# Optimization experiments

Hardware: AMD Instinct MI355X
Metric: run time of the kernel (lower is better)

Reference implementation:

```python
import jax, jax.numpy as jnp
from jax import lax
import numpy as np

COMMITMENT_COST = 0.25
DATA_VARIANCE = 1.0
DN = ('NCHW', 'OIHW', 'NCHW')


def _conv(x, w, b, stride, pad):
    y = lax.conv_general_dilated(x, w, (stride, stride), ((pad, pad), (pad, pad)), dimension_numbers=DN)
    return y + b[None, :, None, None]


def _conv_t(x, w, b, stride, pad, out_pad):
    # PyTorch ConvTranspose2d(w: [Cin, Cout, kH, kW]) == dilated conv with flipped, transposed kernel
    wf = jnp.flip(w, (2, 3)).transpose(1, 0, 2, 3)  # -> [Cout, Cin, kH, kW]
    k = w.shape[2]
    lo, hi = k - 1 - pad, k - 1 - pad + out_pad
    y = lax.conv_general_dilated(x, wf, (1, 1), ((lo, hi), (lo, hi)), lhs_dilation=(stride, stride), dimension_numbers=DN)
    return y + b[None, :, None, None]


def setup_inputs() -> dict:
    key = jax.random.key(0)
    ks = jax.random.split(key, 14)
    n = lambda k, shp, s: (jax.random.normal(k, shp, dtype=jnp.float32) * s)
    return {
        'x': n(ks[0], (64, 3, 256, 256), 1.0),
        'enc_w1': n(ks[1], (32, 3, 3, 3), 0.2), 'enc_b1': n(ks[2], (32,), 0.02),
        'enc_w2': n(ks[3], (64, 32, 3, 3), 0.06), 'enc_b2': n(ks[4], (64,), 0.02),
        'enc_w3': n(ks[5], (16, 64, 1, 1), 0.12), 'enc_b3': n(ks[6], (16,), 0.02),
        'codebook': n(ks[7], (512, 16), 1.0),
        'dec_w1': n(ks[8], (16, 64, 3, 3), 0.08), 'dec_b1': n(ks[9], (64,), 0.02),
        'dec_w2': n(ks[10], (64, 32, 3, 3), 0.04), 'dec_b2': n(ks[11], (32,), 0.02),
        'dec_w3': n(ks[12], (32, 3, 3, 3), 0.06), 'dec_b3': n(ks[13], (3,), 0.02),
    }


def reference(x, enc_w1, enc_b1, enc_w2, enc_b2, enc_w3, enc_b3, codebook,
              dec_w1, dec_b1, dec_w2, dec_b2, dec_w3, dec_b3):
    # Encoder: 3 -> 32 (s2) -> 64 (s2) -> D (1x1)
    z = jax.nn.relu(_conv(x, enc_w1, enc_b1, 2, 1))
    z = jax.nn.relu(_conv(z, enc_w2, enc_b2, 2, 1))
    z = _conv(z, enc_w3, enc_b3, 1, 0)  # [B, D, H/4, W/4]

    # Vector quantization (training path)
    zp = z.transpose(0, 2, 3, 1)                      # [B, h, w, D]
    D = zp.shape[-1]
    flat = zp.reshape(-1, D)                          # [N, D]
    dist = (jnp.sum(flat * flat, axis=1, keepdims=True)
            + jnp.sum(codebook * codebook, axis=1)
            - 2.0 * flat @ codebook.T)                # [N, K]
    idx = jnp.argmin(dist, axis=1)                    # [N]
    quantized = codebook[idx].reshape(zp.shape)       # [B, h, w, D]

    q_latent_loss = jnp.mean((quantized - lax.stop_gradient(zp)) ** 2)
    e_latent_loss = jnp.mean((zp - lax.stop_gradient(quantized)) ** 2)
    e_q_loss = q_latent_loss + COMMITMENT_COST * e_latent_loss

    ste = zp + lax.stop_gradient(quantized - zp)      # straight-through
    e = ste.transpose(0, 3, 1, 2)                     # [B, D, h, w]

    # Decoder: D -> 64 (x2) -> 32 (x2) -> 3
    y = jax.nn.relu(_conv_t(e, dec_w1, dec_b1, 2, 1, 1))
    y = jax.nn.relu(_conv_t(y, dec_w2, dec_b2, 2, 1, 1))
    x_recon = _conv_t(y, dec_w3, dec_b3, 1, 1, 0)

    recon_mse = jnp.mean((x_recon - x) ** 2)
    recon_loss = recon_mse / DATA_VARIANCE
    return jnp.stack([e_q_loss, recon_loss, recon_mse])
```

## Files before the change

kernel.cpp:

```cpp
#include <hip/hip_runtime.h>
#include <hip/hip_bf16.h>


typedef __attribute__((ext_vector_type(8))) short bf16x8;
typedef __attribute__((ext_vector_type(4))) float f32x4;
typedef __attribute__((ext_vector_type(4))) int i32x4;
typedef unsigned short ushort_t;

__device__ __forceinline__ ushort_t f2bf(float v) {
    __hip_bfloat16 h = __float2bfloat16(v);
    return *(ushort_t*)&h;
}
__device__ __forceinline__ float bf2f(ushort_t u) {
    __hip_bfloat16 h = *(__hip_bfloat16*)&u;
    return __bfloat162float(h);
}
__device__ __forceinline__ unsigned pack2r(float a, float b) {
    return (unsigned)f2bf(fmaxf(a, 0.f)) | ((unsigned)f2bf(fmaxf(b, 0.f)) << 16);
}
__device__ __forceinline__ int xcd_chunk(int flat, int nwg) {
    return (flat & 7) * (nwg >> 3) + (flat >> 3);
}
#define ROR_FRAG(dst, src, CTRL)                                        \
    {                                                                   \
        i32x4 _a = __builtin_bit_cast(i32x4, src), _r;                  \
        _r[0] = __builtin_amdgcn_mov_dpp(_a[0], CTRL, 0xF, 0xF, false); \
        _r[1] = __builtin_amdgcn_mov_dpp(_a[1], CTRL, 0xF, 0xF, false); \
        _r[2] = __builtin_amdgcn_mov_dpp(_a[2], CTRL, 0xF, 0xF, false); \
        _r[3] = __builtin_amdgcn_mov_dpp(_a[3], CTRL, 0xF, 0xF, false); \
        dst = __builtin_bit_cast(bf16x8, _r);                           \
    }


__global__ void zero_k(float* __restrict__ acc) {
    acc[blockIdx.x * 256 + threadIdx.x] = 0.f;
}

__global__ __launch_bounds__(256) void prep_k(
        const float* __restrict__ ew1, const float* __restrict__ ew2,
        const float* __restrict__ dw1, const float* __restrict__ dw2,
        const float* __restrict__ dw3, const float* __restrict__ cb,
        ushort_t* __restrict__ wt, float* __restrict__ cn) {
    int idx = blockIdx.x * 256 + threadIdx.x;
    if (idx < 1024) {
        int co = idx >> 5, k = idx & 31;
        wt[idx] = (k < 27) ? f2bf(ew1[co * 27 + k]) : (ushort_t)0;
    } else if (idx < 19456) {
        int i = idx - 1024;
        int t = i >> 11, co = (i >> 5) & 63, ci = i & 31;
        int lci = ((ci & 1) << 4) | (ci >> 1);
        wt[idx] = f2bf(ew2[co * 288 + lci * 9 + t]);
    } else if (idx < 37888) {
        int i = idx - 19456;
        int t = i >> 11, co = (i >> 5) & 63, k = i & 31;
        wt[idx] = (k < 16) ? f2bf(dw1[k * 576 + co * 9 + t]) : (ushort_t)0;
    } else if (idx < 56320) {
        int i = idx - 37888;
        int t = i >> 11, kc = (i >> 10) & 1, co = (i >> 5) & 31, ci = i & 31;
        int m = kc * 32 + ci;
        int lci = ((m & 3) << 4) | (m >> 2);
        wt[idx] = f2bf(dw2[lci * 288 + co * 9 + t]);
    } else if (idx < 60928) {
        int i = idx - 56320;
        int t = i >> 9, co = (i >> 5) & 15, ci = i & 31;
        int lci = ((ci & 1) << 4) | (ci >> 1);
        wt[idx] = (co < 3) ? f2bf(dw3[lci * 27 + co * 9 + (8 - t)]) : (ushort_t)0;
    } else if (idx < 61440) {
        int k = idx - 60928;
        float s = 0.f;
        #pragma unroll
        for (int d = 0; d < 16; ++d) { float v = cb[k * 16 + d]; s += v * v; }
        cn[k] = s;
    }
}

__global__ __launch_bounds__(256) void pad_k(ushort_t* __restrict__ d1p) {
    const int img = blockIdx.x, tid = threadIdx.x;
    const uint4 z = (uint4){0, 0, 0, 0};
    uint4* b1 = (uint4*)(d1p + (size_t)img * 1065024);
    for (int i = tid; i < 1032; i += 256) b1[132096 + i] = z;
    for (int i = tid; i < 1024; i += 256) {
        int r = i >> 3, u = i & 7;
        b1[(r * 129 + 128) * 8 + u] = z;
    }
}

__global__ __launch_bounds__(256, 4) void conv1_k(const float* __restrict__ x,
        const ushort_t* __restrict__ wt, const float* __restrict__ bias,
        ushort_t* __restrict__ a1) {
    const int L = xcd_chunk(blockIdx.y, gridDim.y);
    const int b = L >> 7, oh = L & 127;
    const int tid = threadIdx.x;
    __shared__ __align__(16) ushort_t sX[9 * 264];
    __shared__ int sOff[32];
    for (int i = tid; i < 9 * 264 / 2; i += 256) ((unsigned*)sX)[i] = 0u;
    if (tid < 32) {
        int k = tid, off = 0;
        if (k < 27) { int ci = k / 9, r9 = k % 9, kh = r9 / 3, kw = r9 % 3;
                      off = (ci * 3 + kh) * 264 + kw; }
        sOff[tid] = off;
    }
    __syncthreads();
    #pragma unroll
    for (int it = 0; it < 9; ++it) {
        int slot = it * 256 + tid;
        int ci = slot / 768, r = slot % 768, kh = r >> 8, iw = r & 255;
        int ih = 2 * oh + kh - 1;
        float v = ((unsigned)ih < 256u) ? x[(long)(b * 3 + ci) * 65536 + ih * 256 + iw] : 0.f;
        sX[(ci * 3 + kh) * 264 + iw + 1] = f2bf(v);
    }
    __syncthreads();
    const int lane = tid & 63, wave = tid >> 6, q = lane >> 4, n16 = lane & 15;
    bf16x8 Bw[2];
    #pragma unroll
    for (int u = 0; u < 2; ++u)
        Bw[u] = *(const bf16x8*)(wt + (u * 16 + n16) * 32 + q * 8);
    f32x4 acc[2][2];
    #pragma unroll
    for (int u = 0; u < 2; ++u) {
        float bz = bias[u * 16 + n16];
        acc[0][u] = (f32x4){bz, bz, bz, bz};
        acc[1][u] = (f32x4){bz, bz, bz, bz};
    }
    #pragma unroll
    for (int mf = 0; mf < 2; ++mf) {
        const int m2 = 2 * (wave * 32 + mf * 16 + n16);
        ushort_t av[8];
        #pragma unroll
        for (int j = 0; j < 8; ++j) {
            int k = q * 8 + j;
            av[j] = (k < 27) ? sX[sOff[k] + m2] : (ushort_t)0;
        }
        bf16x8 A = *(bf16x8*)av;
        #pragma unroll
        for (int u = 0; u < 2; ++u)
            acc[mf][u] = __builtin_amdgcn_mfma_f32_16x16x32_bf16(A, Bw[u], acc[mf][u], 0, 0, 0);
    }
    #pragma unroll
    for (int mf = 0; mf < 2; ++mf)
        #pragma unroll
        for (int r = 0; r < 4; ++r) {
            int ow = wave * 32 + mf * 16 + q * 4 + r;
            *(unsigned*)(a1 + ((long)(b * 128 + oh) * 128 + ow) * 32 + n16 * 2) =
                pack2r(acc[mf][0][r], acc[mf][1][r]);
        }
}

__global__ __launch_bounds__(256, 4) void conv2_k(const ushort_t* __restrict__ a1,
        const ushort_t* __restrict__ wt, const float* __restrict__ bias,
        ushort_t* __restrict__ a2) {
    const int L = xcd_chunk(blockIdx.y, gridDim.y);
    const int b = L >> 6, oh = L & 63;
    const int tid = threadIdx.x;
    __shared__ __align__(16) ushort_t sA[3 * 2 * 66 * 40];
    uint4* z4 = (uint4*)sA;
    #pragma unroll
    for (int it = 0; it < 8; ++it) {
        int slot = it * 256 + tid;
        if (slot < 1980) z4[slot] = (uint4){0, 0, 0, 0};
    }
    __syncthreads();
    #pragma unroll
    for (int it = 0; it < 6; ++it) {
        int slot = it * 256 + tid;
        if (slot < 1536) {
            int kh = slot >> 9, rem = slot & 511, iw = rem >> 2, ci8 = (rem & 3) << 3;
            int ih = 2 * oh + kh - 1;
            if ((unsigned)ih < 128u) {
                uint4 v = *(const uint4*)(a1 + ((long)(b * 128 + ih) * 128 + iw) * 32 + ci8);
                int idx = iw + 2, p = idx & 1, c = idx >> 1;
                *(uint4*)&sA[((kh * 2 + p) * 66 + c) * 40 + ci8] = v;
            }
        }
    }
    __syncthreads();
    const int lane = tid & 63, wave = tid >> 6, q = lane >> 4, n16 = lane & 15;
    f32x4 acc[4];
    #pragma unroll
    for (int u = 0; u < 4; ++u) {
        float bz = bias[u * 16 + n16];
        acc[u] = (f32x4){bz, bz, bz, bz};
    }
    const int ow = wave * 16 + n16;
    #pragma unroll
    for (int t = 0; t < 9; ++t) {
        const int kh = t / 3, kw = t % 3;
        const int p = (kw == 1) ? 0 : 1;
        const int c = (kw == 0) ? ow : ow + 1;
        bf16x8 A = *(bf16x8*)&sA[((kh * 2 + p) * 66 + c) * 40 + q * 8];
        #pragma unroll
        for (int u = 0; u < 4; ++u) {
            bf16x8 B = *(const bf16x8*)(wt + 1024 + t * 2048 + (u * 16 + n16) * 32 + q * 8);
            acc[u] = __builtin_amdgcn_mfma_f32_16x16x32_bf16(A, B, acc[u], 0, 0, 0);
        }
    }
    #pragma unroll
    for (int r = 0; r < 4; ++r) {
        int owo = wave * 16 + q * 4 + r;
        uint2 pk;
        pk.x = pack2r(acc[0][r], acc[1][r]);
        pk.y = pack2r(acc[2][r], acc[3][r]);
        *(uint2*)(a2 + ((long)(b * 64 + oh) * 64 + owo) * 64 + n16 * 4) = pk;
    }
}

__global__ __launch_bounds__(256) void conv3_vq_k(const ushort_t* __restrict__ a2,
        const float* __restrict__ w3, const float* __restrict__ b3,
        const float* __restrict__ cb, const float* __restrict__ cn,
        ushort_t* __restrict__ e, float* __restrict__ acc) {
    const int base = blockIdx.x * 512 + threadIdx.x;
    __shared__ float sred[4];
    float z[2][16];
    #pragma unroll
    for (int p = 0; p < 2; ++p)
        #pragma unroll
        for (int d = 0; d < 16; ++d) z[p][d] = b3[d];
    #pragma unroll
    for (int p = 0; p < 2; ++p) {
        const ushort_t* arow = a2 + (long)(base + p * 256) * 64;
        #pragma unroll
        for (int c8 = 0; c8 < 8; ++c8) {
            uint4 raw = *(const uint4*)(arow + c8 * 8);
            ushort_t us[8];
            *(uint4*)us = raw;
            #pragma unroll
            for (int j = 0; j < 8; ++j) {
                int m = c8 * 8 + j;
                int lci = ((m & 3) << 4) | (m >> 2);
                float a = bf2f(us[j]);
                #pragma unroll
                for (int d = 0; d < 16; ++d)
                    z[p][d] = fmaf(a, w3[d * 64 + lci], z[p][d]);
            }
        }
    }
    const float4* cb4 = (const float4*)cb;
    float best0 = 1e30f, best1 = 1e30f; int bi0 = 0, bi1 = 0;
    for (int k = 0; k < 512; ++k) {
        float4 c0 = cb4[k * 4 + 0], c1 = cb4[k * 4 + 1];
        float4 c2 = cb4[k * 4 + 2], c3 = cb4[k * 4 + 3];
        float nk = cn[k];
        float d0 = z[0][0]*c0.x + z[0][1]*c0.y + z[0][2]*c0.z + z[0][3]*c0.w
                 + z[0][4]*c1.x + z[0][5]*c1.y + z[0][6]*c1.z + z[0][7]*c1.w
                 + z[0][8]*c2.x + z[0][9]*c2.y + z[0][10]*c2.z + z[0][11]*c2.w
                 + z[0][12]*c3.x + z[0][13]*c3.y + z[0][14]*c3.z + z[0][15]*c3.w;
        float d1 = z[1][0]*c0.x + z[1][1]*c0.y + z[1][2]*c0.z + z[1][3]*c0.w
                 + z[1][4]*c1.x + z[1][5]*c1.y + z[1][6]*c1.z + z[1][7]*c1.w
                 + z[1][8]*c2.x + z[1][9]*c2.y + z[1][10]*c2.z + z[1][11]*c2.w
                 + z[1][12]*c3.x + z[1][13]*c3.y + z[1][14]*c3.z + z[1][15]*c3.w;
        float dist0 = nk - 2.f * d0, dist1 = nk - 2.f * d1;
        if (dist0 < best0) { best0 = dist0; bi0 = k; }
        if (dist1 < best1) { best1 = dist1; bi1 = k; }
    }
    float lsum = 0.f;
    #pragma unroll
    for (int d = 0; d < 16; ++d) {
        float q0 = cb[bi0 * 16 + d], q1 = cb[bi1 * 16 + d];
        float f0 = q0 - z[0][d], f1 = q1 - z[1][d];
        lsum += f0 * f0 + f1 * f1;
        e[(long)base * 16 + d] = f2bf(q0);
        e[(long)(base + 256) * 16 + d] = f2bf(q1);
    }
    #pragma unroll
    for (int off = 32; off > 0; off >>= 1) lsum += __shfl_down(lsum, off, 64);
    if ((threadIdx.x & 63) == 0) sred[threadIdx.x >> 6] = lsum;
    __syncthreads();
    if (threadIdx.x == 0)
        atomicAdd(&acc[(blockIdx.x & 63) << 5],
                  sred[0] + sred[1] + sred[2] + sred[3]);
}

__global__ __launch_bounds__(256, 4) void dec1_k(const ushort_t* __restrict__ e,
        const ushort_t* __restrict__ wt, const float* __restrict__ bias,
        ushort_t* __restrict__ d1p) {
    const int L = xcd_chunk(blockIdx.y, gridDim.y);
    const int b = L >> 6, i = L & 63;
    const int tid = threadIdx.x;
    __shared__ __align__(16) ushort_t sE[2 * 66 * 24];
    uint4* z4 = (uint4*)sE;
    #pragma unroll
    for (int it = 0; it < 2; ++it) {
        int slot = it * 256 + tid;
        if (slot < 396) z4[slot] = (uint4){0, 0, 0, 0};
    }
    __syncthreads();
    {
        int dh = tid >> 7, rem = tid & 127, j = rem >> 1, ci8 = (rem & 1) * 8;
        if (i + dh < 64) {
            uint4 v = *(const uint4*)(e + ((long)((b * 64 + i + dh) * 64 + j)) * 16 + ci8);
            *(uint4*)&sE[(dh * 66 + j) * 24 + ci8] = v;
        }
    }
    __syncthreads();
    const int lane = tid & 63, wave = tid >> 6, q = lane >> 4, n16 = lane & 15;
    f32x4 acc[4][4];
    #pragma unroll
    for (int u = 0; u < 4; ++u) {
        float bz = bias[u * 16 + n16];
        #pragma unroll
        for (int c = 0; c < 4; ++c) acc[c][u] = (f32x4){bz, bz, bz, bz};
    }
    const int jl = wave * 16 + n16;
    #pragma unroll
    for (int t = 0; t < 9; ++t) {
        const int kh = t / 3, kw = t % 3;
        const int dh = (kh == 0) ? 1 : 0, dw = (kw == 0) ? 1 : 0;
        const int cls = ((kh != 1) ? 2 : 0) | ((kw != 1) ? 1 : 0);
        bf16x8 A = *(bf16x8*)&sE[(dh * 66 + jl + dw) * 24 + (q & 1) * 8];
        #pragma unroll
        for (int u = 0; u < 4; ++u) {
            bf16x8 B = *(const bf16x8*)(wt + 19456 + t * 2048 + (u * 16 + n16) * 32 + q * 8);
            acc[cls][u] = __builtin_amdgcn_mfma_f32_16x16x32_bf16(A, B, acc[cls][u], 0, 0, 0);
        }
    }
    #pragma unroll
    for (int ph = 0; ph < 2; ++ph)
        #pragma unroll
        for (int pw = 0; pw < 2; ++pw)
            #pragma unroll
            for (int r = 0; r < 4; ++r) {
                int oh = 2 * i + ph;
                int ow = 2 * (wave * 16 + q * 4 + r) + pw;
                uint2 pk;
                pk.x = pack2r(acc[ph * 2 + pw][0][r], acc[ph * 2 + pw][1][r]);
                pk.y = pack2r(acc[ph * 2 + pw][2][r], acc[ph * 2 + pw][3][r]);
                *(uint2*)(d1p + (size_t)b * 1065024 + ((long)oh * 129 + ow) * 64 + n16 * 4) = pk;
            }
}

__global__ __launch_bounds__(256, 3) void dec23_k(const ushort_t* __restrict__ d1p,
        const ushort_t* __restrict__ wt, const float* __restrict__ db2,
        const float* __restrict__ db3, const float* __restrict__ x,
        float* __restrict__ acc) {
    const int flat = blockIdx.y * 2 + blockIdx.x;
    const int L = xcd_chunk(flat, gridDim.y * 2);
    const int bx = L & 1, byl = L >> 1;
    const int b = byl >> 6, i4 = byl & 63;
    const int j0 = bx << 7;
    const int tid = threadIdx.x;
    const int lane = tid & 63, wave = tid >> 6, q = lane >> 4, n16 = lane & 15;

    __shared__ __align__(16) ushort_t sT[6 * 132 * 32];
    __shared__ float sred[4];

    {
        unsigned* sw = (unsigned*)sT;
        if (tid < 96) {
            int r6 = tid >> 4, w16 = tid & 15;
            int c = (bx == 0) ? 0 : 129;
            sw[r6 * 2112 + c * 16 + w16] = 0u;
        }
        if (i4 == 0)
            for (int i = tid; i < 2080; i += 256) sw[i] = 0u;
        if (i4 == 63)
            for (int i = tid; i < 2080; i += 256) sw[5 * 2112 + i] = 0u;
    }
    __syncthreads();

    const int bb0 = (j0 >> 1) - 1;
    const ushort_t* dbase = d1p + (size_t)b * 1065024;
    const int aidx = wave;
    const int a = 2 * i4 + aidx - 1;
    const bool doP0 = (aidx != 0);
    const bool doP1 = (aidx != 3);
    int r0 = a, r1 = a + 1;
    r0 = ((unsigned)r0 <= 128u) ? r0 : 128;
    r1 = ((unsigned)r1 <= 128u) ? r1 : 128;
    const ushort_t* rowp0 = dbase + (long)r0 * 8256;
    const ushort_t* rowp1 = dbase + (long)r1 * 8256;
    int colo[5][2];
    #pragma unroll
    for (int cell = 0; cell < 5; ++cell)
        #pragma unroll
        for (int dw = 0; dw < 2; ++dw) {
            int col = bb0 + cell * 16 + n16 + dw;
            colo[cell][dw] = (((unsigned)col <= 128u) ? col : 128) * 64;
        }
    const float bz0 = db2[n16], bz1 = db2[16 + n16];
    f32x4 a5[2][5];

#define INIT5()                                                                     \
    _Pragma("unroll")                                                               \
    for (int cell = 0; cell < 5; ++cell) {                                          \
        a5[0][cell] = (f32x4){bz0, bz0, bz0, bz0};                                  \
        a5[1][cell] = (f32x4){bz1, bz1, bz1, bz1};                                  \
    }
#define TAP5(T, DH, DW)                                                             \
    {                                                                               \
        const ushort_t* wb = wt + 37888 + (T) * 2048;                               \
        const ushort_t* rp = (DH) ? rowp1 : rowp0;                                  \
        _Pragma("unroll")                                                           \
        for (int kc = 0; kc < 2; ++kc) {                                            \
            bf16x8 B0 = *(const bf16x8*)(wb + kc * 1024 + n16 * 32 + q * 8);        \
            bf16x8 B1 = *(const bf16x8*)(wb + kc * 1024 + (16 + n16) * 32 + q * 8); \
            _Pragma("unroll")                                                       \
            for (int cell = 0; cell < 5; ++cell) {                                  \
                bf16x8 Av = *(const bf16x8*)(rp + colo[cell][DW] + kc * 32 + q * 8);\
                a5[0][cell] = __builtin_amdgcn_mfma_f32_16x16x32_bf16(              \
                    Av, B0, a5[0][cell], 0, 0, 0);                                  \
                a5[1][cell] = __builtin_amdgcn_mfma_f32_16x16x32_bf16(              \
                    Av, B1, a5[1][cell], 0, 0, 0);                                  \
            }                                                                       \
        }                                                                           \
    }
#define EPI5(PH, PW)                                                                \
    {                                                                               \
        int R = 2 * a + (PH);                                                       \
        if ((unsigned)R < 256u) {                                                   \
            int Rp = R - 4 * i4 + 1;                                                \
            _Pragma("unroll")                                                       \
            for (int cell = 0; cell < 5; ++cell)                                    \
                _Pragma("unroll")                                                   \
                for (int r = 0; r < 4; ++r) {                                       \
                    int lq = cell * 16 + q * 4 + r;                                 \
                    int cp = 2 * lq + (PW) - 1;                                     \
                    int cg = 2 * (bb0 + lq) + (PW);                                 \
                    if ((unsigned)cg < 256u && (unsigned)cp < 130u)                 \
                        *(unsigned*)&sT[Rp * 4224 + cp * 32 + n16 * 2] =            \
                            pack2r(a5[0][cell][r], a5[1][cell][r]);                 \
                }                                                                   \
        }                                                                           \
    }
    if (doP0) {
        INIT5(); TAP5(4, 0, 0); EPI5(0, 0);
        INIT5(); TAP5(3, 0, 1); TAP5(5, 0, 0); EPI5(0, 1);
    }
    if (doP1) {
        INIT5(); TAP5(1, 1, 0); TAP5(7, 0, 0); EPI5(1, 0);
        INIT5(); TAP5(0, 1, 1); TAP5(2, 1, 0); TAP5(6, 0, 1); TAP5(8, 0, 0);
        EPI5(1, 1);
    }
#undef INIT5
#undef TAP5
#undef EPI5
    __syncthreads();

    float bz3 = (n16 < 3) ? db3[n16] : 0.f;
    f32x4 a4[8];
    #pragma unroll
    for (int mf = 0; mf < 8; ++mf) a4[mf] = (f32x4){bz3, bz3, bz3, bz3};
    const int oh = 4 * i4 + wave;
    const bool is_l0 = (n16 == 0), is_l15 = (n16 == 15);
    #pragma unroll
    for (int kh = 0; kh < 3; ++kh) {
        const ushort_t* srow = &sT[(wave + kh) * 4224];
        bf16x8 Bk0 = *(const bf16x8*)(wt + 56320 + (kh * 3 + 0) * 512 + n16 * 32 + q * 8);
        bf16x8 Bk1 = *(const bf16x8*)(wt + 56320 + (kh * 3 + 1) * 512 + n16 * 32 + q * 8);
        bf16x8 Bk2 = *(const bf16x8*)(wt + 56320 + (kh * 3 + 2) * 512 + n16 * 32 + q * 8);
        bf16x8 G[8];
        #pragma unroll
        for (int mf = 0; mf < 8; ++mf)
            G[mf] = *(const bf16x8*)(srow + (mf * 16 + n16 + 1) * 32 + q * 8);
        bf16x8 E  = *(const bf16x8*)(srow + n16 * 32 + q * 8);
        bf16x8 E2 = *(const bf16x8*)(srow + (114 + n16) * 32 + q * 8);
        #pragma unroll
        for (int mf = 0; mf < 8; ++mf)
            a4[mf] = __builtin_amdgcn_mfma_f32_16x16x32_bf16(G[mf], Bk1, a4[mf], 0, 0, 0);
        bf16x8 P = E;
        #pragma unroll
        for (int mf = 0; mf < 8; ++mf) {
            bf16x8 Qm; ROR_FRAG(Qm, G[mf], 0x121);
            bf16x8 kw0 = is_l0 ? P : Qm;
            a4[mf] = __builtin_amdgcn_mfma_f32_16x16x32_bf16(kw0, Bk0, a4[mf], 0, 0, 0);
            P = Qm;
        }
        P = E2;
        #pragma unroll
        for (int mf = 7; mf >= 0; --mf) {
            bf16x8 Rm; ROR_FRAG(Rm, G[mf], 0x12F);
            bf16x8 kw2 = is_l15 ? P : Rm;
            a4[mf] = __builtin_amdgcn_mfma_f32_16x16x32_bf16(kw2, Bk2, a4[mf], 0, 0, 0);
            P = Rm;
        }
    }
    float lsum = 0.f;
    if (n16 < 3) {
        const float* xrow = x + ((long)(b * 3 + n16) * 256 + oh) * 256 + j0;
        #pragma unroll
        for (int mf = 0; mf < 8; ++mf)
            #pragma unroll
            for (int r = 0; r < 4; ++r) {
                int ow = mf * 16 + q * 4 + r;
                float df = a4[mf][r] - xrow[ow];
                lsum += df * df;
            }
    }
    #pragma unroll
    for (int off = 32; off > 0; off >>= 1) lsum += __shfl_down(lsum, off, 64);
    if (lane == 0) sred[wave] = lsum;
    __syncthreads();
    if (tid == 0)
        atomicAdd(&acc[2048 + ((byl & 63) << 5)],
                  sred[0] + sred[1] + sred[2] + sred[3]);
}

__global__ void finalize_k(const float* __restrict__ acc, float* __restrict__ out) {
    int t = threadIdx.x;
    float v = acc[t << 5];
    float m = acc[2048 + (t << 5)];
    #pragma unroll
    for (int off = 32; off > 0; off >>= 1) {
        v += __shfl_down(v, off, 64);
        m += __shfl_down(m, off, 64);
    }
    if (t == 0) {
        float eq  = 1.25f * v / 4194304.f;
        float mse = m / 12582912.f;
        out[0] = eq;
        out[1] = mse;
        out[2] = mse;
    }
}

extern "C" void kernel_launch(void* const* d_in, const int* in_sizes, int n_in,
                              void* d_out, int out_size, void* d_ws, size_t ws_size,
                              hipStream_t stream) {
    (void)in_sizes; (void)n_in; (void)out_size;
    const float* x   = (const float*)d_in[0];
    const float* ew1 = (const float*)d_in[1];
    const float* eb1 = (const float*)d_in[2];
    const float* ew2 = (const float*)d_in[3];
    const float* eb2 = (const float*)d_in[4];
    const float* ew3 = (const float*)d_in[5];
    const float* eb3 = (const float*)d_in[6];
    const float* cb  = (const float*)d_in[7];
    const float* dw1 = (const float*)d_in[8];
    const float* db1 = (const float*)d_in[9];
    const float* dw2 = (const float*)d_in[10];
    const float* db2 = (const float*)d_in[11];
    const float* dw3 = (const float*)d_in[12];
    const float* db3 = (const float*)d_in[13];
    float* out = (float*)d_out;

    int C = 64;
    while (C > 1 && (size_t)147456 + (size_t)C * 2261120UL > ws_size) C >>= 1;

    char* base = (char*)d_ws;
    float*    acc = (float*)base;
    ushort_t* wt  = (ushort_t*)(base + 16384);
    float*    cn  = (float*)(base + 16384 + 121856);
    ushort_t* e   = (ushort_t*)(base + 147456);
    char*     rgn = base + 147456 + (size_t)C * 131072UL;
    ushort_t* a1  = (ushort_t*)rgn;
    ushort_t* a2  = (ushort_t*)(rgn + (size_t)C * 1048576UL);
    ushort_t* d1p = (ushort_t*)rgn;

    zero_k<<<16, 256, 0, stream>>>(acc);
    prep_k<<<240, 256, 0, stream>>>(ew1, ew2, dw1, dw2, dw3, cb, wt, cn);

    for (int b0 = 0; b0 < 64; b0 += C) {
        const float* xc = x + (size_t)b0 * 196608UL;
        conv1_k   <<<dim3(1, C * 128), 256, 0, stream>>>(xc,  wt, eb1, a1);
        conv2_k   <<<dim3(1, C * 64),  256, 0, stream>>>(a1,  wt, eb2, a2);
        conv3_vq_k<<<dim3(C * 8),      256, 0, stream>>>(a2,  ew3, eb3, cb, cn, e, acc);
        pad_k     <<<dim3(C),          256, 0, stream>>>(d1p);
        dec1_k    <<<dim3(1, C * 64),  256, 0, stream>>>(e,   wt, db1, d1p);
        dec23_k   <<<dim3(2, C * 64),  256, 0, stream>>>(d1p, wt, db2, db3, xc, acc);
    }
    finalize_k<<<1, 64, 0, stream>>>(acc, out);
}
```

Before: 652.7 us.

## Reorder deconv2 loops cell-outer to reuse loaded A fragments across phases

Restructures the second transposed-conv stage so the outer loop is over column cells rather than output phases. Each cell's input fragments (2 rows × 2 column shifts × 2 k-chunks) are loaded once and reused across all four sub-pixel phases and their taps, instead of being reloaded per tap. This cuts repeated A-operand global/cache loads and lowers accumulator register pressure (two accumulators instead of ten). In exchange, weight B fragments are now reloaded once per cell, five times as many weight loads.

```diff
diff --git a/kernel.cpp b/kernel.cpp
--- a/kernel.cpp
+++ b/kernel.cpp
@@ -363,76 +363,97 @@
     const int a = 2 * i4 + aidx - 1;
     const bool doP0 = (aidx != 0);
     const bool doP1 = (aidx != 3);
-    int r0 = a, r1 = a + 1;
-    r0 = ((unsigned)r0 <= 128u) ? r0 : 128;
-    r1 = ((unsigned)r1 <= 128u) ? r1 : 128;
-    const ushort_t* rowp0 = dbase + (long)r0 * 8256;
-    const ushort_t* rowp1 = dbase + (long)r1 * 8256;
-    int colo[5][2];
-    #pragma unroll
-    for (int cell = 0; cell < 5; ++cell)
-        #pragma unroll
-        for (int dw = 0; dw < 2; ++dw) {
-            int col = bb0 + cell * 16 + n16 + dw;
-            colo[cell][dw] = (((unsigned)col <= 128u) ? col : 128) * 64;
-        }
+    int r0 = ((unsigned)a <= 128u) ? a : 128;
+    int r1 = ((unsigned)(a + 1) <= 128u) ? (a + 1) : 128;
+    const ushort_t* rowp[2] = { dbase + (long)r0 * 8256, dbase + (long)r1 * 8256 };
     const float bz0 = db2[n16], bz1 = db2[16 + n16];
-    f32x4 a5[2][5];
-
-#define INIT5()                                                                     \
+
+#define BL(B, T)                                                                    \
     _Pragma("unroll")                                                               \
-    for (int cell = 0; cell < 5; ++cell) {                                          \
-        a5[0][cell] = (f32x4){bz0, bz0, bz0, bz0};                                  \
-        a5[1][cell] = (f32x4){bz1, bz1, bz1, bz1};                                  \
-    }
-#define TAP5(T, DH, DW)                                                             \
-    {                                                                               \
-        const ushort_t* wb = wt + 37888 + (T) * 2048;                               \
-        const ushort_t* rp = (DH) ? rowp1 : rowp0;                                  \
+    for (int kc = 0; kc < 2; ++kc)                                                  \
         _Pragma("unroll")                                                           \
-        for (int kc = 0; kc < 2; ++kc) {                                            \
-            bf16x8 B0 = *(const bf16x8*)(wb + kc * 1024 + n16 * 32 + q * 8);        \
-            bf16x8 B1 = *(const bf16x8*)(wb + kc * 1024 + (16 + n16) * 32 + q * 8); \
-            _Pragma("unroll")                                                       \
-            for (int cell = 0; cell < 5; ++cell) {                                  \
-                bf16x8 Av = *(const bf16x8*)(rp + colo[cell][DW] + kc * 32 + q * 8);\
-                a5[0][cell] = __builtin_amdgcn_mfma_f32_16x16x32_bf16(              \
-                    Av, B0, a5[0][cell], 0, 0, 0);                                  \
-                a5[1][cell] = __builtin_amdgcn_mfma_f32_16x16x32_bf16(              \
-                    Av, B1, a5[1][cell], 0, 0, 0);                                  \
-            }                                                                       \
-        }                                                                           \
-    }
-#define EPI5(PH, PW)                                                                \
+        for (int u = 0; u < 2; ++u)                                                 \
+            B[kc][u] = *(const bf16x8*)(wt + 37888 + (T) * 2048 + kc * 1024         \
+                                        + (u * 16 + n16) * 32 + q * 8);
+#define MAC(c0v, c1v, DH, DW, B)                                                    \
+    c0v = __builtin_amdgcn_mfma_f32_16x16x32_bf16(A8[0][DH][DW], B[0][0], c0v, 0, 0, 0); \
+    c1v = __builtin_amdgcn_mfma_f32_16x16x32_bf16(A8[0][DH][DW], B[0][1], c1v, 0, 0, 0); \
+    c0v = __builtin_amdgcn_mfma_f32_16x16x32_bf16(A8[1][DH][DW], B[1][0], c0v, 0, 0, 0); \
+    c1v = __builtin_amdgcn_mfma_f32_16x16x32_bf16(A8[1][DH][DW], B[1][1], c1v, 0, 0, 0);
+#define EPI(cell, PH, PW, c0v, c1v)                                                 \
     {                                                                               \
         int R = 2 * a + (PH);                                                       \
         if ((unsigned)R < 256u) {                                                   \
             int Rp = R - 4 * i4 + 1;                                                \
             _Pragma("unroll")                                                       \
-            for (int cell = 0; cell < 5; ++cell)                                    \
-                _Pragma("unroll")                                                   \
-                for (int r = 0; r < 4; ++r) {                                       \
-                    int lq = cell * 16 + q * 4 + r;                                 \
-                    int cp = 2 * lq + (PW) - 1;                                     \
-                    int cg = 2 * (bb0 + lq) + (PW);                                 \
-                    if ((unsigned)cg < 256u && (unsigned)cp < 130u)                 \
-                        *(unsigned*)&sT[Rp * 4224 + cp * 32 + n16 * 2] =            \
-                            pack2r(a5[0][cell][r], a5[1][cell][r]);                 \
-                }                                                                   \
+            for (int r = 0; r < 4; ++r) {                                           \
+                int lq = (cell) * 16 + q * 4 + r;                                   \
+                int cp = 2 * lq + (PW) - 1;                                         \
+                int cg = 2 * (bb0 + lq) + (PW);                                     \
+                if ((unsigned)cg < 256u && (unsigned)cp < 130u)                     \
+                    *(unsigned*)&sT[Rp * 4224 + cp * 32 + n16 * 2] =                \
+                        pack2r(c0v[r], c1v[r]);                                     \
+            }                                                                       \
         }                                                                           \
     }
-    if (doP0) {
-        INIT5(); TAP5(4, 0, 0); EPI5(0, 0);
-        INIT5(); TAP5(3, 0, 1); TAP5(5, 0, 0); EPI5(0, 1);
-    }
-    if (doP1) {
-        INIT5(); TAP5(1, 1, 0); TAP5(7, 0, 0); EPI5(1, 0);
-        INIT5(); TAP5(0, 1, 1); TAP5(2, 1, 0); TAP5(6, 0, 1); TAP5(8, 0, 0);
-        EPI5(1, 1);
-    }
-#undef INIT5
-#undef TAP5
-#undef EPI5
+#define CELL(cell)                                                                  \
+    {                                                                               \
+        int ca = bb0 + (cell) * 16 + n16;                                           \
+        int o0 = (((unsigned)ca <= 128u) ? ca : 128) * 64;                          \
+        int cbn = ca + 1;                                                           \
+        int o1 = (((unsigned)cbn <= 128u) ? cbn : 128) * 64;                        \
+        bf16x8 A8[2][2][2];                   \
+        _Pragma("unroll")                                                           \
+        for (int kc = 0; kc < 2; ++kc)                                              \
+            _Pragma("unroll")                                                       \
+            for (int dh = 0; dh < 2; ++dh) {                                        \
+                A8[kc][dh][0] = *(const bf16x8*)(rowp[dh] + o0 + kc * 32 + q * 8);  \
+                A8[kc][dh][1] = *(const bf16x8*)(rowp[dh] + o1 + kc * 32 + q * 8);  \
+            }                                                                       \
+        if (doP0) {                                                                 \
+            {   bf16x8 Bt[2][2]; BL(Bt, 4)                                          \
+                f32x4 c0 = (f32x4){bz0, bz0, bz0, bz0};                             \
+                f32x4 c1 = (f32x4){bz1, bz1, bz1, bz1};                             \
+                MAC(c0, c1, 0, 0, Bt)                                               \
+                EPI(cell, 0, 0, c0, c1)                                             \
+            }                                                                       \
+            {   bf16x8 B3[2][2]; BL(B3, 3)                                          \
+                bf16x8 B5[2][2]; BL(B5, 5)                                          \
+                f32x4 c0 = (f32x4){bz0, bz0, bz0, bz0};                             \
+                f32x4 c1 = (f32x4){bz1, bz1, bz1, bz1};                             \
+                MAC(c0, c1, 0, 1, B3)                                               \
+                MAC(c0, c1, 0, 0, B5)                                               \
+                EPI(cell, 0, 1, c0, c1)                                             \
+            }                                                                       \
+        }                                                                           \
+        if (doP1) {                                                                 \
+            {   bf16x8 B1[2][2]; BL(B1, 1)                                          \
+                bf16x8 B7[2][2]; BL(B7, 7)                                          \
+                f32x4 c0 = (f32x4){bz0, bz0, bz0, bz0};                             \
+                f32x4 c1 = (f32x4){bz1, bz1, bz1, bz1};                             \
+                MAC(c0, c1, 1, 0, B1)                                               \
+                MAC(c0, c1, 0, 0, B7)                                               \
+                EPI(cell, 1, 0, c0, c1)                                             \
+            }                                                                       \
+            {   bf16x8 B0[2][2]; BL(B0, 0)                                          \
+                bf16x8 B2[2][2]; BL(B2, 2)                                          \
+                bf16x8 B6[2][2]; BL(B6, 6)                                          \
+                bf16x8 B8[2][2]; BL(B8, 8)                                          \
+                f32x4 c0 = (f32x4){bz0, bz0, bz0, bz0};                             \
+                f32x4 c1 = (f32x4){bz1, bz1, bz1, bz1};                             \
+                MAC(c0, c1, 1, 1, B0)                                               \
+                MAC(c0, c1, 1, 0, B2)                                               \
+                MAC(c0, c1, 0, 1, B6)                                               \
+                MAC(c0, c1, 0, 0, B8)                                               \
+                EPI(cell, 1, 1, c0, c1)                                             \
+            }                                                                       \
+        }                                                                           \
+    }
+    CELL(0) CELL(1) CELL(2) CELL(3) CELL(4)
+#undef BL
+#undef MAC
+#undef EPI
+#undef CELL
     __syncthreads();
 
     float bz3 = (n16 < 3) ? db3[n16] : 0.f;
```

New measurement: 782.0 us. 19.8% more time.
